# Kernel tuning notes

Measured on AMD Instinct MI355X. Metric: run time of the kernel, lower is better.

Reference implementation:

```python
import jax, jax.numpy as jnp
import numpy as np

NUM_EMBEDDINGS = 1024
EMBEDDING_DIM = 256
COMMITMENT_COST = 0.25


def setup_inputs() -> dict:
    key = jax.random.key(0)
    k1, k2 = jax.random.split(key)
    inputs = jax.random.normal(k1, (32, EMBEDDING_DIM, 32, 32), dtype=jnp.float32)
    # torch init: uniform_(-1/K, 1/K)
    emb_w = jax.random.uniform(k2, (NUM_EMBEDDINGS, EMBEDDING_DIM), dtype=jnp.float32,
                               minval=-1.0 / NUM_EMBEDDINGS, maxval=1.0 / NUM_EMBEDDINGS)
    return {"inputs": inputs, "emb_w": emb_w}


def reference(inputs, emb_w):
    sg = jax.lax.stop_gradient
    # BCHW -> BHWC
    x = jnp.transpose(inputs, (0, 2, 3, 1))
    in_shape = x.shape
    flat = x.reshape(-1, EMBEDDING_DIM)  # [N, D]
    # squared L2 distances to codebook: [N, K]
    distances = (jnp.sum(flat * flat, axis=1, keepdims=True)
                 + jnp.sum(emb_w * emb_w, axis=1)
                 - 2.0 * jnp.matmul(flat, emb_w.T))
    idx = jnp.argmin(distances, axis=1)  # [N]
    encodings = jax.nn.one_hot(idx, NUM_EMBEDDINGS, dtype=jnp.float32)  # [N, K]
    # one-hot @ codebook == gather
    quantized = jnp.take(emb_w, idx, axis=0).reshape(in_shape)  # [B,H,W,D]
    e_latent_loss = jnp.mean((sg(quantized) - x) ** 2)
    q_latent_loss = jnp.mean((quantized - sg(x)) ** 2)
    loss = q_latent_loss + COMMITMENT_COST * e_latent_loss
    # straight-through estimator
    quantized_st = x + sg(quantized - x)
    avg_probs = jnp.mean(encodings, axis=0)
    perplexity = jnp.exp(-jnp.sum(avg_probs * jnp.log(avg_probs + 1e-10)))
    return (loss, jnp.transpose(quantized_st, (0, 3, 1, 2)), perplexity, encodings)
```

## Files before the change

### kernel.cpp

```cpp
#include <hip/hip_runtime.h>
#include <hip/hip_bf16.h>

typedef short short8 __attribute__((ext_vector_type(8)));
typedef float f32x4 __attribute__((ext_vector_type(4)));
typedef unsigned short u16x4 __attribute__((ext_vector_type(4)));

#define D_ 256
#define K_ 1024
#define HW_ 1024
#define NROWS_ 32768
#define QELEMS 8388608
#define NBLK_ (NROWS_ / 64)

static __device__ __forceinline__ unsigned short to_bf16(float v) {
    __hip_bfloat16 h = __float2bfloat16(v);
    return *(unsigned short*)&h;
}

__global__ __launch_bounds__(256) void vq_prep(const float* __restrict__ emb,
    unsigned short* __restrict__ ebf2, float* __restrict__ enorm,
    int* __restrict__ counts, double* __restrict__ loss_acc)
{
    __shared__ float part[256];
    const int ct = blockIdx.x, t = threadIdx.x;
    const int col = t & 15, s = t >> 4;
    const int k = ct * 16 + col;
    const f32x4* src = (const f32x4*)(emb + (size_t)k * D_ + s * 16);
    short8 f0, f1;
    float a = 0.f;
#pragma unroll
    for (int j = 0; j < 4; ++j) {
        f32x4 v = src[j];
#pragma unroll
        for (int q = 0; q < 4; ++q) {
            int idx = j * 4 + q;
            unsigned short h = to_bf16(v[q]);
            a = fmaf(v[q], v[q], a);
            if (idx < 8) f0[idx] = (short)h; else f1[idx - 8] = (short)h;
        }
    }
    part[t] = a;
    char* base = (char*)ebf2 + ct * 8192 + (s >> 1) * 1024 + ((s & 1) * 2) * 256 + col * 16;
    *(short8*)base = f0;
    *(short8*)(base + 256) = f1;
    __syncthreads();
    if (t < 16) {
        float s2 = 0.f;
#pragma unroll
        for (int j = 0; j < 16; ++j) s2 += part[t + 16 * j];
        enorm[ct * 16 + t] = s2;
    }
    if (ct < 4) counts[ct * 256 + t] = 0;
    if (ct == 0 && t == 0) *loss_acc = 0.0;
}

__global__ __launch_bounds__(512, 4) void vq_main(
    const float* __restrict__ x, const float* __restrict__ emb,
    const unsigned short* __restrict__ ebf2, const float* __restrict__ enorm,
    int* __restrict__ counts, double* __restrict__ loss_acc, float* __restrict__ out)
{
    __shared__ char smem[65536];
    __shared__ float xn[64][9];
    __shared__ float rminv[64][4];
    __shared__ int   rmini[64][4];
    __shared__ int   bestsh[64];

    char* xs = smem;
    char* es = smem;

    const int t = threadIdx.x;
    const int n0 = blockIdx.x * 64;
    const int b = n0 >> 10;
    const int hw0 = n0 & 1023;
    const float* xbase = x + (size_t)b * (D_ * HW_) + hw0;

    {
        const int rt = t & 15, r0 = rt * 4;
        const int dg = t >> 4;
        float xp[4] = {0.f, 0.f, 0.f, 0.f};
#pragma unroll
        for (int m = 0; m < 2; ++m) {
            int d0 = (dg + 32 * m) * 4;
            f32x4 c[4];
#pragma unroll
            for (int q = 0; q < 4; ++q)
                c[q] = *(const f32x4*)(xbase + (size_t)(d0 + q) * HW_ + r0);
            const int dc = d0 >> 5, kg = (d0 >> 3) & 3, off = (d0 & 7) * 2;
#pragma unroll
            for (int i = 0; i < 4; ++i) {
                u16x4 pk;
                pk[0] = to_bf16(c[0][i]); pk[1] = to_bf16(c[1][i]);
                pk[2] = to_bf16(c[2][i]); pk[3] = to_bf16(c[3][i]);
                xp[i] = fmaf(c[0][i], c[0][i], xp[i]);
                xp[i] = fmaf(c[1][i], c[1][i], xp[i]);
                xp[i] = fmaf(c[2][i], c[2][i], xp[i]);
                xp[i] = fmaf(c[3][i], c[3][i], xp[i]);
                int r = r0 + i;
                int byte = ((r >> 4) << 13) + (dc << 10) + (kg << 8) + ((r & 15) << 4) + off;
                *(u16x4*)(xs + byte) = pk;
            }
        }
#pragma unroll
        for (int i = 0; i < 4; ++i) {
            xp[i] += __shfl_down(xp[i], 32);
            xp[i] += __shfl_down(xp[i], 16);
        }
        if ((t & 48) == 0) {
            int w0 = t >> 6;
#pragma unroll
            for (int i = 0; i < 4; ++i) xn[r0 + i][w0] = xp[i];
        }
    }

    const int lane = t & 63;
    const int w = t >> 6;
    const int rh = w & 1;
    const int cq = w >> 1;
    const int col = lane & 15;
    const char* eb = (const char*)ebf2;
    const int wbyte = w * 4096;

    __syncthreads();

#pragma unroll
    for (int j = 0; j < 4; ++j)
        __builtin_amdgcn_global_load_lds(eb + wbyte + j * 1024 + lane * 16,
                                         es + 32768 + wbyte + j * 1024, 16, 0, 0);

    short8 areg[2][8];
#pragma unroll
    for (int rt = 0; rt < 2; ++rt) {
        const char* ab = xs + ((rh * 2 + rt) << 13);
#pragma unroll
        for (int dc = 0; dc < 8; ++dc)
            areg[rt][dc] = *(const short8*)(ab + dc * 1024 + lane * 16);
    }

    float v1[8]; int i1[8];
#pragma unroll
    for (int s = 0; s < 8; ++s) { v1[s] = 3.4e38f; i1[s] = 0x7fffffff; }

    for (int cc = 0; cc < 16; ++cc) {
        __syncthreads();
        const int hc = ((cc & 1) ^ 1) * 32768;
        if (cc < 15) {
            const char* src = eb + (size_t)(cc + 1) * 32768;
            const int hn = (cc & 1) * 32768;
#pragma unroll
            for (int j = 0; j < 4; ++j)
                __builtin_amdgcn_global_load_lds(src + wbyte + j * 1024 + lane * 16,
                                                 es + hn + wbyte + j * 1024, 16, 0, 0);
        }
        const char* tb = es + hc + (cq << 13);
        f32x4 acc0 = {0.f, 0.f, 0.f, 0.f};
        f32x4 acc1 = {0.f, 0.f, 0.f, 0.f};
#pragma unroll
        for (int dc = 0; dc < 8; ++dc) {
            short8 bf = *(const short8*)(tb + dc * 1024 + lane * 16);
            acc0 = __builtin_amdgcn_mfma_f32_16x16x32_bf16(areg[0][dc], bf, acc0, 0, 0, 0);
            acc1 = __builtin_amdgcn_mfma_f32_16x16x32_bf16(areg[1][dc], bf, acc1, 0, 0, 0);
        }
        const int code = cc * 64 + cq * 16 + col;
        const float bn = enorm[code];
#pragma unroll
        for (int r = 0; r < 4; ++r) {
            float dv = fmaf(-2.f, acc0[r], bn);
            if (dv < v1[r]) { v1[r] = dv; i1[r] = code; }
            float dw = fmaf(-2.f, acc1[r], bn);
            if (dw < v1[4 + r]) { v1[4 + r] = dw; i1[4 + r] = code; }
        }
    }

#pragma unroll
    for (int mask = 1; mask < 16; mask <<= 1) {
#pragma unroll
        for (int s = 0; s < 8; ++s) {
            float ov = __shfl_xor(v1[s], mask);
            int oi = __shfl_xor(i1[s], mask);
            if (ov < v1[s] || (ov == v1[s] && oi < i1[s])) { v1[s] = ov; i1[s] = oi; }
        }
    }
    {
        const int kg = lane >> 4;
        if (col == 0) {
#pragma unroll
            for (int s = 0; s < 8; ++s) {
                int rt = s >> 2, r = s & 3;
                int row = rh * 32 + rt * 16 + kg * 4 + r;
                rminv[row][cq] = v1[s];
                rmini[row][cq] = i1[s];
            }
        }
    }
    __syncthreads();

    if (t < 64) {
        float dmin = rminv[t][0]; int best = rmini[t][0];
#pragma unroll
        for (int g = 1; g < 4; ++g) {
            float cv = rminv[t][g]; int ci = rmini[t][g];
            if (cv < dmin || (cv == dmin && ci < best)) { dmin = cv; best = ci; }
        }
        bestsh[t] = best;
        atomicAdd(&counts[best], 1);
        float s = 0.f;
#pragma unroll
        for (int g = 0; g < 8; ++g) s += xn[t][g];
        float lrow = dmin + s;
        for (int o = 32; o > 0; o >>= 1) lrow += __shfl_down(lrow, o);
        if (t == 0) atomicAdd(loss_acc, (double)lrow);
    }
    __syncthreads();

    {
        int r = w * 8 + (lane >> 3);
        int c = lane & 7;
        const f32x4* src4 = (const f32x4*)emb + (size_t)bestsh[r] * 64;
        float* q = (float*)smem + r * 256;
        int xr = r & 31;
#pragma unroll
        for (int j = 0; j < 8; ++j) {
            f32x4 v = src4[8 * j + c];
#pragma unroll
            for (int kq = 0; kq < 4; ++kq) {
                int d = 4 * (8 * j + c) + kq;
                q[d ^ xr] = v[kq];
            }
        }
    }
    __syncthreads();

    {
        const int hwr = t & 63;
        const int dq = t >> 6;
        float* outq = out + 1 + (size_t)b * (D_ * HW_) + hw0 + hwr;
        const float* q = (const float*)smem + hwr * 256;
        int xr = hwr & 31;
#pragma unroll
        for (int dd = 0; dd < 32; ++dd) {
            int d = dq + dd * 8;
            outq[(size_t)d * HW_] = q[d ^ xr];
        }
    }
    {
        float2* ez = (float2*)(out + 8388610 + (size_t)(n0 + w * 8) * 1024);
        const float2 zz = {0.f, 0.f};
#pragma unroll 8
        for (int j = 0; j < 64; ++j) ez[j * 64 + lane] = zz;
    }
    __syncthreads();
    if (t < 64) out[8388610 + (size_t)(n0 + t) * 1024 + bestsh[t]] = 1.0f;
}

__global__ __launch_bounds__(256) void vq_fin(const int* __restrict__ counts,
    const double* __restrict__ loss_acc, float* __restrict__ d_out)
{
    int t = threadIdx.x;
    double s = 0.0;
    for (int k = t; k < K_; k += 256) {
        double p = (double)counts[k] / 32768.0;
        s += p * log(p + 1e-10);
    }
    for (int o = 32; o > 0; o >>= 1) s += __shfl_down(s, o);
    __shared__ double sred[4];
    if ((t & 63) == 0) sred[t >> 6] = s;
    __syncthreads();
    if (t == 0) {
        double tot = sred[0] + sred[1] + sred[2] + sred[3];
        d_out[0] = (float)(1.25 * (*loss_acc) / (double)QELEMS);
        d_out[8388609] = (float)exp(-tot);
    }
}

extern "C" void kernel_launch(void* const* d_in, const int* in_sizes, int n_in,
                              void* d_out, int out_size, void* d_ws, size_t ws_size,
                              hipStream_t stream)
{
    const float* x = (const float*)d_in[0];
    const float* emb = (const float*)d_in[1];
    char* ws = (char*)d_ws;
    unsigned short* ebf2 = (unsigned short*)(ws);
    float* enorm = (float*)(ws + 524288);
    int* counts = (int*)(ws + 528384);
    double* lacc = (double*)(ws + 532480);
    float* out = (float*)d_out;

    vq_prep<<<64, 256, 0, stream>>>(emb, ebf2, enorm, counts, lacc);
    vq_main<<<NBLK_, 512, 0, stream>>>(x, emb, ebf2, enorm, counts, lacc, out);
    vq_fin<<<1, 256, 0, stream>>>(counts, lacc, out);
}
```

Measured before the change: 68.87 us.

## Load codebook tiles straight to registers and interleave one-hot zeroing into loop

Drops the double-buffered LDS staging of the bf16 codebook. Each wave now loads its MFMA B-fragments directly from global memory (served from L2/cache), which removes the per-iteration block-wide barrier. Zeroing of the one-hot encodings output moves into the distance loop so those stores overlap with MFMA work, and the trailing barrier is dropped. The cost is duplicated global traffic for codebook fragments (wave pairs reload the same tile) and longer load latency exposed to each wave.

```diff
diff --git a/kernel.cpp b/kernel.cpp
--- a/kernel.cpp
+++ b/kernel.cpp
@@ -66,7 +66,6 @@
     __shared__ int   bestsh[64];
 
     char* xs = smem;
-    char* es = smem;
 
     const int t = threadIdx.x;
     const int n0 = blockIdx.x * 64;
@@ -118,14 +117,8 @@
     const int cq = w >> 1;
     const int col = lane & 15;
     const char* eb = (const char*)ebf2;
-    const int wbyte = w * 4096;
-
-    __syncthreads();
-
-#pragma unroll
-    for (int j = 0; j < 4; ++j)
-        __builtin_amdgcn_global_load_lds(eb + wbyte + j * 1024 + lane * 16,
-                                         es + 32768 + wbyte + j * 1024, 16, 0, 0);
+
+    __syncthreads();
 
     short8 areg[2][8];
 #pragma unroll
@@ -140,25 +133,21 @@
 #pragma unroll
     for (int s = 0; s < 8; ++s) { v1[s] = 3.4e38f; i1[s] = 0x7fffffff; }
 
+    float2* ezw = (float2*)(out + 8388610 + (size_t)(n0 + w * 8) * 1024);
+    const float2 zz = {0.f, 0.f};
+
     for (int cc = 0; cc < 16; ++cc) {
-        __syncthreads();
-        const int hc = ((cc & 1) ^ 1) * 32768;
-        if (cc < 15) {
-            const char* src = eb + (size_t)(cc + 1) * 32768;
-            const int hn = (cc & 1) * 32768;
-#pragma unroll
-            for (int j = 0; j < 4; ++j)
-                __builtin_amdgcn_global_load_lds(src + wbyte + j * 1024 + lane * 16,
-                                                 es + hn + wbyte + j * 1024, 16, 0, 0);
-        }
-        const char* tb = es + hc + (cq << 13);
+        const char* tb = eb + cc * 32768 + (cq << 13);
+        short8 bf[8];
+#pragma unroll
+        for (int dc = 0; dc < 8; ++dc)
+            bf[dc] = *(const short8*)(tb + dc * 1024 + lane * 16);
         f32x4 acc0 = {0.f, 0.f, 0.f, 0.f};
         f32x4 acc1 = {0.f, 0.f, 0.f, 0.f};
 #pragma unroll
         for (int dc = 0; dc < 8; ++dc) {
-            short8 bf = *(const short8*)(tb + dc * 1024 + lane * 16);
-            acc0 = __builtin_amdgcn_mfma_f32_16x16x32_bf16(areg[0][dc], bf, acc0, 0, 0, 0);
-            acc1 = __builtin_amdgcn_mfma_f32_16x16x32_bf16(areg[1][dc], bf, acc1, 0, 0, 0);
+            acc0 = __builtin_amdgcn_mfma_f32_16x16x32_bf16(areg[0][dc], bf[dc], acc0, 0, 0, 0);
+            acc1 = __builtin_amdgcn_mfma_f32_16x16x32_bf16(areg[1][dc], bf[dc], acc1, 0, 0, 0);
         }
         const int code = cc * 64 + cq * 16 + col;
         const float bn = enorm[code];
@@ -169,6 +158,9 @@
             float dw = fmaf(-2.f, acc1[r], bn);
             if (dw < v1[4 + r]) { v1[4 + r] = dw; i1[4 + r] = code; }
         }
+        float2* ez = ezw + cc * 256;
+#pragma unroll
+        for (int j = 0; j < 4; ++j) ez[j * 64 + lane] = zz;
     }
 
 #pragma unroll
@@ -242,13 +234,6 @@
             outq[(size_t)d * HW_] = q[d ^ xr];
         }
     }
-    {
-        float2* ez = (float2*)(out + 8388610 + (size_t)(n0 + w * 8) * 1024);
-        const float2 zz = {0.f, 0.f};
-#pragma unroll 8
-        for (int j = 0; j < 64; ++j) ez[j * 64 + lane] = zz;
-    }
-    __syncthreads();
     if (t < 64) out[8388610 + (size_t)(n0 + t) * 1024 + bestsh[t]] = 1.0f;
 }
 
```

After: 62.44 us. 9.3% less time.
